# Performance work log

Hardware: AMD Instinct MI355X
Metric: run time of the kernel (lower is better)

The kernel has to match this reference:

```python
import jax, jax.numpy as jnp
import numpy as np

D = 256
N = 1024
L = 6
H = 4
NAMES = ['self', 'cross', 'self', 'cross', 'self', 'cross']


def setup_inputs() -> dict:
    key = jax.random.key(0)
    ks = jax.random.split(key, 12)
    f32 = jnp.float32
    s = D ** -0.5
    s2 = (2 * D) ** -0.5
    return {
        'desc0': jax.random.normal(ks[0], (1, D, N), f32),
        'desc1': jax.random.normal(ks[1], (1, D, N), f32),
        'desc2': jax.random.normal(ks[2], (1, D, N), f32),
        'desc3': jax.random.normal(ks[3], (1, D, N), f32),
        'dist': jax.random.uniform(ks[4], (1, N, N), f32),
        'unreachable': jnp.zeros((N, N), dtype=bool),
        'fidx': jax.random.randint(ks[5], (N, 2), 0, 100),
        'lmb': jax.random.randint(ks[6], (8, 4), 0, 100),
        'proj_w': jax.random.normal(ks[7], (3, L, 3, D, D), f32) * s,
        'proj_b': jnp.zeros((3, L, 3, D), f32),
        'merge_w': jax.random.normal(ks[8], (3, L, D, D), f32) * s,
        'merge_b': jnp.zeros((3, L, D), f32),
        'mlp_w1': jax.random.normal(ks[9], (3, L, 2 * D, 2 * D), f32) * s2,
        'mlp_b1': jnp.zeros((3, L, 2 * D), f32),
        'mlp_w2': jax.random.normal(ks[10], (3, L, D, 2 * D), f32) * s2,
        'mlp_b2': jnp.zeros((3, L, D), f32),
        'norm_g': jnp.ones((4, L, D), f32),
        'norm_b': jnp.zeros((4, L, D), f32),
    }


def _conv(w, b, x):
    # Conv1d kernel_size=1 == per-position linear over channel dim. x: [1, Cin, N]
    return jnp.einsum('od,bdn->bon', w, x) + b[None, :, None]


def _ln(x, g, b):
    # torch does LayerNorm(D) on x.transpose(1,2); equivalent to normalizing channel dim of [1, D, N]
    mu = jnp.mean(x, axis=1, keepdims=True)
    var = jnp.var(x, axis=1, keepdims=True)
    xn = (x - mu) * jax.lax.rsqrt(var + 1e-5)
    return xn * g[None, :, None] + b[None, :, None]


def _mha(pw, pb, mw, mb, q, k, v):
    # pw: [3, D, D], pb: [3, D]; q/k/v: [1, D, Nq/Nk/Nk]; mask is always None in this model
    dh = D // H
    qh = _conv(pw[0], pb[0], q).reshape(1, dh, H, -1)  # [1, dh, H, Nq]
    kh = _conv(pw[1], pb[1], k).reshape(1, dh, H, -1)
    vh = _conv(pw[2], pb[2], v).reshape(1, dh, H, -1)
    scores = jnp.einsum('bdhn,bdhm->bhnm', qh, kh) / jnp.asarray(dh, q.dtype) ** 0.5
    prob = jax.nn.softmax(scores, axis=-1)
    x = jnp.einsum('bhnm,bdhm->bdhn', prob, vh)  # [1, dh, H, Nq]
    out = _conv(mw, mb, x.reshape(1, D, -1))
    return out, scores.mean(axis=1)  # weights: [1, Nq, Nk]


def reference(desc0, desc1, desc2, desc3, dist, unreachable, fidx, lmb,
              proj_w, proj_b, merge_w, merge_b, mlp_w1, mlp_b1, mlp_w2, mlp_b2,
              norm_g, norm_b):
    # ablation == 0 path; dist, fidx, lmb feed dead code in the original forward.
    def prop(br, i, x, src):
        msg, wts = _mha(proj_w[br, i], proj_b[br, i], merge_w[br, i], merge_b[br, i], x, src, src)
        h = jnp.concatenate([x, msg], axis=1)  # [1, 2D, N]
        h = jax.nn.relu(_conv(mlp_w1[br, i], mlp_b1[br, i], h))
        return _conv(mlp_w2[br, i], mlp_b2[br, i], h), wts

    d0, d1, d2, d3 = desc0, desc1, desc2, desc3
    score1 = None
    for i, name in enumerate(NAMES):
        if name == 'cross':
            src0, src1 = d1, d0
        else:
            src0, src1 = d0, d1
        delta0, _ = prop(0, i, d0, src0)
        delta1, score1 = prop(0, i, d1, src1)
        if name == 'cross':
            delta21, _ = prop(1, i, d2, d1)
            delta12, _ = prop(1, i, d1, d2)
            d2 = _ln(d2 + delta21, norm_g[2, i], norm_b[2, i])
            delta03, _ = prop(2, i, d0, d3)
            delta30, _ = prop(2, i, d3, d0)
            d3 = _ln(d3 + delta30, norm_g[3, i], norm_b[3, i])
            d0 = d0 + delta0 + delta03
            d1 = d1 + delta1 + delta12
        else:
            delta2, _ = prop(1, i, d2, d2)
            d2 = _ln(d2 + delta2, norm_g[2, i], norm_b[2, i])
            delta3, _ = prop(2, i, d3, d3)
            d3 = _ln(d3 + delta3, norm_g[3, i], norm_b[3, i])
            d0 = d0 + delta0
            d1 = d1 + delta1
        d0 = _ln(d0, norm_g[0, i], norm_b[0, i])
        d1 = _ln(d1, norm_g[1, i], norm_b[1, i])

    scores = score1.mean(axis=1).reshape(-1)  # [N0]
    unreachable_frontiers = jnp.any(unreachable, axis=0)  # [N0]
    return jnp.where(unreachable_frontiers, jnp.asarray(-1e9, scores.dtype), scores)
```

## Files before the change

kernel.cpp:

```cpp
#include <hip/hip_runtime.h>

#define D 256
#define NPTS 1024
#define H 4
#define LNUM 6

static constexpr size_t SL = (size_t)D * NPTS;

typedef __attribute__((ext_vector_type(8))) short bf16x8;
typedef __attribute__((ext_vector_type(4))) float f32x4;

__device__ __forceinline__ unsigned f2bf(float f) {
  unsigned u = __float_as_uint(f);
  return (u + 0x7FFFu + ((u >> 16) & 1u)) >> 16;
}
__device__ __forceinline__ unsigned pack2(float a, float b) {
  return f2bf(a) | (f2bf(b) << 16);
}
__device__ __forceinline__ float bf2f(unsigned u) {
  return __uint_as_float(u << 16);
}
__device__ __forceinline__ int swz(int row, int byteInRow) {
  return row * 128 + (byteInRow ^ ((row & 7) << 4));
}

struct MMArgs {
  const unsigned short* X[18];
  const unsigned short* X2[18];
  const unsigned short* W[18];
  const float* B[18];
  void* O[18];
};

template <bool RELU>
__global__ __launch_bounds__(256) void mm_bf16(MMArgs a, int K, int xs, int os,
                                               int mode0, int qkv, int split) {
  const int z = blockIdx.z;
  const unsigned short* __restrict__ X = a.X[z];
  const unsigned short* __restrict__ X2 = a.X2[z];
  const unsigned short* __restrict__ W = a.W[z];
  const float* __restrict__ Bb = a.B[z];

  int mode = mode0, osz = os;
  if (qkv && (z % 3 == 2)) { mode = 2; osz = 1024; }
  const float osc = (qkv && (z % 3 == 0)) ? 0.125f : 1.0f;

  __shared__ char sm[64 * 68 * 4];
  char* smX = sm;
  char* smW = sm + 8192;

  const int tid = threadIdx.x;
  const int n0 = blockIdx.x * 64, m0 = blockIdx.y * 64;
  const int lane = tid & 63, wid = tid >> 6;

  f32x4 acc[4] = {{0.f, 0.f, 0.f, 0.f}, {0.f, 0.f, 0.f, 0.f},
                  {0.f, 0.f, 0.f, 0.f}, {0.f, 0.f, 0.f, 0.f}};

  const int srow = tid >> 3, skb = (tid & 7) * 16;
  const int ar = wid * 16 + (lane & 15);
  const int kh = (lane >> 4) * 16;

  for (int k0 = 0; k0 < K; k0 += 64) {
    const int kw = k0 + (skb >> 1);
    int kx = kw;
    const unsigned short* xsrc = X;
    if (split && kx >= split) { xsrc = X2; kx -= split; }
#pragma unroll
    for (int p = 0; p < 2; ++p) {
      const int row = srow + 32 * p;
      *(float4*)(smX + swz(row, skb)) =
          *(const float4*)(xsrc + (size_t)(n0 + row) * xs + kx);
      *(float4*)(smW + swz(row, skb)) =
          *(const float4*)(W + (size_t)(m0 + row) * K + kw);
    }
    __syncthreads();
    const bf16x8 a0 = *(const bf16x8*)(smX + swz(ar, kh));
    const bf16x8 a1 = *(const bf16x8*)(smX + swz(ar, 64 + kh));
#pragma unroll
    for (int c = 0; c < 4; ++c) {
      const int br = c * 16 + (lane & 15);
      const bf16x8 b0 = *(const bf16x8*)(smW + swz(br, kh));
      const bf16x8 b1 = *(const bf16x8*)(smW + swz(br, 64 + kh));
      acc[c] = __builtin_amdgcn_mfma_f32_16x16x32_bf16(a0, b0, acc[c], 0, 0, 0);
      acc[c] = __builtin_amdgcn_mfma_f32_16x16x32_bf16(a1, b1, acc[c], 0, 0, 0);
    }
    __syncthreads();
  }

  float(*eps)[68] = (float(*)[68])sm;
#pragma unroll
  for (int c = 0; c < 4; ++c) {
    const float bs = Bb[m0 + c * 16 + (lane & 15)];
#pragma unroll
    for (int r = 0; r < 4; ++r) {
      float v = (acc[c][r] + bs) * osc;
      if (RELU) v = fmaxf(v, 0.f);
      eps[wid * 16 + (lane >> 4) * 4 + r][c * 16 + (lane & 15)] = v;
    }
  }
  __syncthreads();

#pragma unroll
  for (int p = 0; p < 2; ++p) {
    const int row = srow + 32 * p;
    const int c0 = (tid & 7) * 8;
    if (mode == 0) {
      const float4 lo = *(const float4*)&eps[row][c0];
      const float4 hi = *(const float4*)&eps[row][c0 + 4];
      uint4 u = {pack2(lo.x, lo.y), pack2(lo.z, lo.w), pack2(hi.x, hi.y), pack2(hi.z, hi.w)};
      *(uint4*)((unsigned short*)a.O[z] + (size_t)(n0 + row) * osz + m0 + c0) = u;
    } else if (mode == 1) {
      float* O = (float*)a.O[z];
      *(float4*)(O + (size_t)(n0 + row) * osz + m0 + c0) = *(const float4*)&eps[row][c0];
      *(float4*)(O + (size_t)(n0 + row) * osz + m0 + c0 + 4) = *(const float4*)&eps[row][c0 + 4];
    } else {
      float v[8];
#pragma unroll
      for (int j = 0; j < 8; ++j) v[j] = eps[c0 + j][row];
      uint4 u = {pack2(v[0], v[1]), pack2(v[2], v[3]), pack2(v[4], v[5]), pack2(v[6], v[7])};
      *(uint4*)((unsigned short*)a.O[z] + (size_t)(m0 + row) * osz + n0 + c0) = u;
    }
  }
}

struct AttnArgs {
  const unsigned short* Q[6];
  const unsigned short* K[6];
  const unsigned short* V[6];
};

__global__ __launch_bounds__(256) void attn_split(AttnArgs a, unsigned short* part) {
  const int z = blockIdx.z;
  const int h = blockIdx.y >> 2, ck = blockIdx.y & 3;
  const int n0 = blockIdx.x * 64;
  const unsigned short* __restrict__ Qp = a.Q[z];
  const unsigned short* __restrict__ Kp = a.K[z];
  const unsigned short* __restrict__ Vp = a.V[z];

  __shared__ char sm[49152];
  char* smQ = sm;
  char* smKb = sm + 8192;
  char* smVb = sm + 24576;
  char* smP = sm + 40960;

  const int tid = threadIdx.x;
  const int lane = tid & 63, wid = tid >> 6;
  const int srow = tid >> 2, skb = (tid & 3) * 16;
  const int kb0 = ck * 256;

#pragma unroll
  for (int p = 0; p < 2; ++p) {
    const int b = skb + 64 * p;
    *(float4*)(smQ + swz(srow, b)) =
        *(const float4*)(Qp + (size_t)(n0 + srow) * 256 + h * 64 + (b >> 1));
    *(float4*)(smKb + swz(srow, b)) =
        *(const float4*)(Kp + (size_t)(kb0 + srow) * 256 + h * 64 + (b >> 1));
    *(float4*)(smVb + swz(srow, b)) =
        *(const float4*)(Vp + (size_t)(h * 64 + srow) * NPTS + kb0 + (b >> 1));
  }
  __syncthreads();

  const int kh = (lane >> 4) * 16;
  const int qr = wid * 16 + (lane & 15);
  const bf16x8 qb0 = *(const bf16x8*)(smQ + swz(qr, kh));
  const bf16x8 qb1 = *(const bf16x8*)(smQ + swz(qr, 64 + kh));

  f32x4 accO[4] = {{0.f, 0.f, 0.f, 0.f}, {0.f, 0.f, 0.f, 0.f},
                   {0.f, 0.f, 0.f, 0.f}, {0.f, 0.f, 0.f, 0.f}};
  float mrun = -1e30f, lrun = 0.f;

  for (int t = 0; t < 4; ++t) {
    const int co = (t & 1) << 13;
    if (t < 3) {
      const int no = ((t + 1) & 1) << 13;
      const int kt = kb0 + (t + 1) * 64;
#pragma unroll
      for (int p = 0; p < 2; ++p) {
        const int b = skb + 64 * p;
        *(float4*)(smKb + no + swz(srow, b)) =
            *(const float4*)(Kp + (size_t)(kt + srow) * 256 + h * 64 + (b >> 1));
        *(float4*)(smVb + no + swz(srow, b)) =
            *(const float4*)(Vp + (size_t)(h * 64 + srow) * NPTS + kt + (b >> 1));
      }
    }

    f32x4 s[4];
#pragma unroll
    for (int c = 0; c < 4; ++c) {
      const int br = c * 16 + (lane & 15);
      const bf16x8 kf0 = *(const bf16x8*)(smKb + co + swz(br, kh));
      const bf16x8 kf1 = *(const bf16x8*)(smKb + co + swz(br, 64 + kh));
      f32x4 tt = {0.f, 0.f, 0.f, 0.f};
      tt = __builtin_amdgcn_mfma_f32_16x16x32_bf16(kf0, qb0, tt, 0, 0, 0);
      tt = __builtin_amdgcn_mfma_f32_16x16x32_bf16(kf1, qb1, tt, 0, 0, 0);
      s[c] = tt;
    }

    float mx = s[0][0];
#pragma unroll
    for (int c = 0; c < 4; ++c)
#pragma unroll
      for (int r = 0; r < 4; ++r) mx = fmaxf(mx, s[c][r]);
    mx = fmaxf(mx, __shfl_xor(mx, 16));
    mx = fmaxf(mx, __shfl_xor(mx, 32));
    const float mn = fmaxf(mrun, mx);
    const float corr = __expf(mrun - mn);
    mrun = mn;
    float ps = 0.f;
#pragma unroll
    for (int c = 0; c < 4; ++c)
#pragma unroll
      for (int r = 0; r < 4; ++r) {
        const float e = __expf(s[c][r] - mn);
        s[c][r] = e;
        ps += e;
      }
    ps += __shfl_xor(ps, 16);
    ps += __shfl_xor(ps, 32);
    lrun = lrun * corr + ps;

#pragma unroll
    for (int c = 0; c < 4; ++c) {
      uint2 u;
      u.x = pack2(s[c][0], s[c][1]);
      u.y = pack2(s[c][2], s[c][3]);
      *(uint2*)(smP + swz(qr, c * 32 + (lane >> 4) * 8)) = u;
    }

#pragma unroll
    for (int r = 0; r < 4; ++r) {
      const float cr = __shfl(corr, ((lane >> 4) & 3) * 4 + r);
#pragma unroll
      for (int c = 0; c < 4; ++c) accO[c][r] *= cr;
    }

    const bf16x8 pa0 = *(const bf16x8*)(smP + swz(qr, kh));
    const bf16x8 pa1 = *(const bf16x8*)(smP + swz(qr, 64 + kh));
#pragma unroll
    for (int c = 0; c < 4; ++c) {
      const int vr = c * 16 + (lane & 15);
      const bf16x8 vb0 = *(const bf16x8*)(smVb + co + swz(vr, kh));
      const bf16x8 vb1 = *(const bf16x8*)(smVb + co + swz(vr, 64 + kh));
      accO[c] = __builtin_amdgcn_mfma_f32_16x16x32_bf16(pa0, vb0, accO[c], 0, 0, 0);
      accO[c] = __builtin_amdgcn_mfma_f32_16x16x32_bf16(pa1, vb1, accO[c], 0, 0, 0);
    }
    __syncthreads();
  }

  char* rec = (char*)part +
              (size_t)((((z * 4 + h) * 16 + blockIdx.x) * 4 + ck)) * 8704;
#pragma unroll
  for (int c = 0; c < 4; ++c)
#pragma unroll
    for (int r = 0; r < 4; ++r) {
      const float o0 = accO[c][r];
      const float o1 = __shfl_xor(o0, 1);
      if (!(lane & 1)) {
        const int row = wid * 16 + (lane >> 4) * 4 + r;
        const int col = c * 16 + (lane & 15);
        *(unsigned*)(rec + row * 128 + col * 2) = pack2(o0, o1);
      }
    }
  if (lane < 16) {
    *(float*)(rec + 8192 + (wid * 16 + lane) * 4) = mrun;
    *(float*)(rec + 8448 + (wid * 16 + lane) * 4) = lrun;
  }
}

struct CmbArgs {
  unsigned short* O[6];
};

__global__ __launch_bounds__(256) void attn_combine(CmbArgs a,
                                                    const unsigned short* part) {
  const int z = blockIdx.z, h = blockIdx.y, qb = blockIdx.x;
  const int tid = threadIdx.x;
  const int q = tid >> 2, t4 = tid & 3;
  const char* base = (const char*)part + (size_t)(((z * 4 + h) * 16 + qb) * 4) * 8704;

  float m[4], l[4];
#pragma unroll
  for (int i = 0; i < 4; ++i) {
    m[i] = *(const float*)(base + i * 8704 + 8192 + q * 4);
    l[i] = *(const float*)(base + i * 8704 + 8448 + q * 4);
  }
  const float M = fmaxf(fmaxf(m[0], m[1]), fmaxf(m[2], m[3]));
  float w[4], L = 0.f;
#pragma unroll
  for (int i = 0; i < 4; ++i) { w[i] = __expf(m[i] - M); L += w[i] * l[i]; }
  const float invL = 1.f / L;

  float o[16] = {};
#pragma unroll
  for (int i = 0; i < 4; ++i) {
    const char* Or = base + i * 8704 + q * 128 + t4 * 32;
    unsigned ua[8];
    *(uint4*)ua = *(const uint4*)Or;
    *(uint4*)(ua + 4) = *(const uint4*)(Or + 16);
#pragma unroll
    for (int j = 0; j < 8; ++j) {
      o[2 * j] += w[i] * bf2f(ua[j] & 0xFFFFu);
      o[2 * j + 1] += w[i] * bf2f(ua[j] >> 16);
    }
  }
  unsigned ou[8];
#pragma unroll
  for (int j = 0; j < 8; ++j) ou[j] = pack2(o[2 * j] * invL, o[2 * j + 1] * invL);
  unsigned short* Op = a.O[z] + (size_t)(qb * 64 + q) * 256 + h * 64 + t4 * 16;
  *(uint4*)Op = *(uint4*)ou;
  *(uint4*)(Op + 8) = *(uint4*)(ou + 4);
}

struct LnArgs {
  float* x[4];
  unsigned short* xb[4];
  const float* da[4];
  const float* db[4];
  const float* g[4];
  const float* b[4];
};

__global__ __launch_bounds__(256) void ln_rows(LnArgs a) {
  const int z = blockIdx.z;
  float* __restrict__ x = a.x[z];
  unsigned short* __restrict__ xb = a.xb[z];
  const float* __restrict__ da = a.da[z];
  const float* __restrict__ db = a.db[z];
  const float* __restrict__ g = a.g[z];
  const float* __restrict__ b = a.b[z];

  const int lane = threadIdx.x & 63, wid = threadIdx.x >> 6;
  const int n = blockIdx.x * 4 + wid;
  const size_t off = (size_t)n * 256 + lane * 4;

  float4 v = *(const float4*)(x + off);
  if (da) {
    const float4 w = *(const float4*)(da + off);
    v.x += w.x; v.y += w.y; v.z += w.z; v.w += w.w;
  }
  if (db) {
    const float4 w = *(const float4*)(db + off);
    v.x += w.x; v.y += w.y; v.z += w.z; v.w += w.w;
  }
  float s = v.x + v.y + v.z + v.w;
  float q = v.x * v.x + v.y * v.y + v.z * v.z + v.w * v.w;
#pragma unroll
  for (int o = 1; o < 64; o <<= 1) {
    s += __shfl_xor(s, o);
    q += __shfl_xor(q, o);
  }
  const float mu = s * (1.f / 256.f);
  const float var = q * (1.f / 256.f) - mu * mu;
  const float inv = rsqrtf(var + 1e-5f);
  const float4 gv = *(const float4*)(g + lane * 4);
  const float4 bv = *(const float4*)(b + lane * 4);
  float4 o;
  o.x = (v.x - mu) * inv * gv.x + bv.x;
  o.y = (v.y - mu) * inv * gv.y + bv.y;
  o.z = (v.z - mu) * inv * gv.z + bv.z;
  o.w = (v.w - mu) * inv * gv.w + bv.w;
  *(float4*)(x + off) = o;
  uint2 pk = {pack2(o.x, o.y), pack2(o.z, o.w)};
  *(uint2*)(xb + off) = pk;
}

struct TrArgs {
  const float* s[4];
  float* d[4];
  unsigned short* db[4];
};
__global__ __launch_bounds__(256) void tr_init(TrArgs a) {
  const int z = blockIdx.z;
  const int n0 = blockIdx.x * 64, c0 = blockIdx.y * 64;
  __shared__ float T[64][65];
  const int tid = threadIdx.x;
#pragma unroll
  for (int p = 0; p < 4; ++p) {
    const int row = (tid >> 4) + 16 * p;
    const int col4 = (tid & 15) * 4;
    const float4 v = *(const float4*)(a.s[z] + (size_t)(c0 + row) * NPTS + n0 + col4);
    T[row][col4] = v.x; T[row][col4 + 1] = v.y; T[row][col4 + 2] = v.z; T[row][col4 + 3] = v.w;
  }
  __syncthreads();
#pragma unroll
  for (int p = 0; p < 4; ++p) {
    const int nr = (tid >> 4) + 16 * p;
    const int c4 = (tid & 15) * 4;
    float4 v;
    v.x = T[c4][nr]; v.y = T[c4 + 1][nr]; v.z = T[c4 + 2][nr]; v.w = T[c4 + 3][nr];
    *(float4*)(a.d[z] + (size_t)(n0 + nr) * 256 + c0 + c4) = v;
    uint2 pk = {pack2(v.x, v.y), pack2(v.z, v.w)};
    *(uint2*)(a.db[z] + (size_t)(n0 + nr) * 256 + c0 + c4) = pk;
  }
}

__global__ __launch_bounds__(256) void wp_qkv(const float* __restrict__ pw,
                                              const float* __restrict__ pb,
                                              unsigned short* __restrict__ wbf,
                                              float* __restrict__ pbias) {
  const int z = blockIdx.z;
  const int pi = z / 3, j = z % 3;
  const int br = pi / 5, i = pi % 5;
  const float* src = pw + (((size_t)br * LNUM + i) * 3 + j) * 65536;
  unsigned short* dst = wbf + (size_t)pi * 655360 + (size_t)j * 65536;
  const int t = blockIdx.x * 256 + threadIdx.x;
  const int mp = t >> 6, k4 = (t & 63) * 4;
  const int m = (mp & 63) * 4 + (mp >> 6);
  const float4 v = *(const float4*)(src + (size_t)m * 256 + k4);
  uint2 pk = {pack2(v.x, v.y), pack2(v.z, v.w)};
  *(uint2*)(dst + (size_t)mp * 256 + k4) = pk;
  if (blockIdx.x == 0) {
    const float* sb = pb + (((size_t)br * LNUM + i) * 3 + j) * 256;
    const int mb = threadIdx.x;
    pbias[(size_t)z * 256 + mb] = sb[(mb & 63) * 4 + (mb >> 6)];
  }
}

__global__ __launch_bounds__(256) void wp_mwt(const float* __restrict__ mw,
                                              unsigned short* __restrict__ wbf,
                                              float* __restrict__ zb) {
  const int pi = blockIdx.z;
  const int br = pi / 5, i = pi % 5;
  const float* src = mw + ((size_t)br * LNUM + i) * 65536;
  unsigned short* dst = wbf + (size_t)pi * 655360 + 196608;
  const int t = blockIdx.x * 256 + threadIdx.x;
  const int cp = t >> 6, m4 = (t & 63) * 4;
  const int c = (cp & 63) * 4 + (cp >> 6);
  float v[4];
#pragma unroll
  for (int u = 0; u < 4; ++u) v[u] = src[(size_t)(m4 + u) * 256 + c];
  uint2 pk = {pack2(v[0], v[1]), pack2(v[2], v[3])};
  *(uint2*)(dst + (size_t)cp * 256 + m4) = pk;
  if (blockIdx.x == 0 && pi == 0) zb[threadIdx.x] = 0.f;
}

__global__ __launch_bounds__(256) void wp_c1(const float* __restrict__ w1,
                                             unsigned short* __restrict__ wbf,
                                             unsigned short* __restrict__ whi) {
  const int pi = blockIdx.z;
  const int br = pi / 5, i = pi % 5;
  const float* src = w1 + ((size_t)br * LNUM + i) * 262144;
  unsigned short* dst = wbf + (size_t)pi * 655360 + 262144;
  const int t = blockIdx.x * 256 + threadIdx.x;
  const float4 v = *(const float4*)(src + (size_t)t * 4);
  uint2 pk = {pack2(v.x, v.y), pack2(v.z, v.w)};
  *(uint2*)(dst + (size_t)t * 4) = pk;
  const int idx = t * 4, row = idx >> 9, col = idx & 511;
  if (col >= 256)
    *(uint2*)(whi + (size_t)pi * 131072 + (size_t)row * 256 + (col - 256)) = pk;
}

__global__ __launch_bounds__(256) void wp_c2(const float* __restrict__ w2,
                                             unsigned short* __restrict__ wbf) {
  const int pi = blockIdx.z;
  const int br = pi / 5, i = pi % 5;
  const float* src = w2 + ((size_t)br * LNUM + i) * 131072;
  unsigned short* dst = wbf + (size_t)pi * 655360 + 524288;
  const int t = blockIdx.x * 256 + threadIdx.x;
  const float4 v = *(const float4*)(src + (size_t)t * 4);
  uint2 pk = {pack2(v.x, v.y), pack2(v.z, v.w)};
  *(uint2*)(dst + (size_t)t * 4) = pk;
}

__global__ __launch_bounds__(256) void b1fold(const float* __restrict__ w1,
                                              const float* __restrict__ mb,
                                              const float* __restrict__ b1,
                                              float* __restrict__ out) {
  const int pi = blockIdx.z;
  const int br = pi / 5, i = pi % 5;
  const float* Wp = w1 + ((size_t)br * LNUM + i) * 262144;
  const float* Bp = mb + ((size_t)br * LNUM + i) * 256;
  const float* b1s = b1 + ((size_t)br * LNUM + i) * 512;
  __shared__ float mbs[256];
  mbs[threadIdx.x] = Bp[threadIdx.x];
  __syncthreads();
  for (int o = threadIdx.x; o < 512; o += 256) {
    float s = b1s[o];
    const float* Wr = Wp + (size_t)o * 512 + 256;
#pragma unroll 4
    for (int m = 0; m < 256; ++m) s = fmaf(Wr[m], mbs[m], s);
    out[(size_t)pi * 512 + o] = s;
  }
}

__device__ __forceinline__ float block_reduce_sum(float v) {
  __shared__ float smr[4];
  const int lane = threadIdx.x & 63, wid = threadIdx.x >> 6;
#pragma unroll
  for (int off = 32; off; off >>= 1) v += __shfl_xor(v, off);
  if (lane == 0) smr[wid] = v;
  __syncthreads();
  if (threadIdx.x == 0) v = smr[0] + smr[1] + smr[2] + smr[3];
  return v;
}

__global__ __launch_bounds__(256) void cs1(const float* __restrict__ X,
                                           float* __restrict__ part) {
  const int r0 = blockIdx.x * 64;
  float acc = 0.f;
  for (int r = 0; r < 64; ++r) acc += X[(size_t)(r0 + r) * 256 + threadIdx.x];
  part[(size_t)blockIdx.x * 256 + threadIdx.x] = acc;
}
__global__ __launch_bounds__(256) void cs2(const float* __restrict__ part,
                                           float* __restrict__ s1) {
  float acc = 0.f;
  for (int b = 0; b < 16; ++b) acc += part[(size_t)b * 256 + threadIdx.x];
  s1[threadIdx.x] = acc;
}
__global__ __launch_bounds__(256) void matvec_qbar(const float* __restrict__ Wq,
                                                   const float* __restrict__ bq,
                                                   const float* __restrict__ s1,
                                                   float* __restrict__ qbar) {
  const int d = blockIdx.x, t = threadIdx.x;
  float s = Wq[(size_t)d * 256 + t] * s1[t];
  s = block_reduce_sum(s);
  if (t == 0) qbar[d] = s + (float)NPTS * bq[d];
}
__global__ __launch_bounds__(256) void matvec_u(const float* __restrict__ Wk,
                                                const float* __restrict__ bk,
                                                const float* __restrict__ qbar,
                                                float* __restrict__ u) {
  const int c = blockIdx.x, t = threadIdx.x;
  float s = (c < 256) ? (Wk[(size_t)t * 256 + c] * qbar[t]) : (bk[t] * qbar[t]);
  s = block_reduce_sum(s);
  if (t == 0) u[c] = s;
}

__global__ __launch_bounds__(256) void ur_or(const unsigned* __restrict__ U,
                                             unsigned* __restrict__ part) {
  const int b = blockIdx.x;
  unsigned o = 0;
  for (int r = 0; r < 16; ++r) o |= U[(size_t)(b * 16 + r) * 256 + threadIdx.x];
  part[(size_t)b * 256 + threadIdx.x] = o;
}

__global__ __launch_bounds__(256) void final2(const float* __restrict__ d0,
                                              const float* __restrict__ u,
                                              const unsigned* __restrict__ part,
                                              float* __restrict__ out) {
  const int lane = threadIdx.x & 63, wid = threadIdx.x >> 6;
  const int m = blockIdx.x * 4 + wid;
  const float4 v = *(const float4*)(d0 + (size_t)m * 256 + lane * 4);
  const float4 uu = *(const float4*)(u + lane * 4);
  float s = v.x * uu.x + v.y * uu.y + v.z * uu.z + v.w * uu.w;
  unsigned f = part[(size_t)lane * 256 + (m >> 2)];
  f = (f >> ((m & 3) * 8)) & 0xFFu;
#pragma unroll
  for (int o = 32; o; o >>= 1) {
    s += __shfl_xor(s, o);
    f |= (unsigned)__shfl_xor((int)f, o);
  }
  if (lane == 0) out[m] = f ? -1e9f : (s + u[256]) * (1.f / 32768.f);
}

extern "C" void kernel_launch(void* const* d_in, const int* in_sizes, int n_in,
                              void* d_out, int out_size, void* d_ws, size_t ws_size,
                              hipStream_t stream) {
  const float* desc[4] = {(const float*)d_in[0], (const float*)d_in[1],
                          (const float*)d_in[2], (const float*)d_in[3]};
  const unsigned char* unreach = (const unsigned char*)d_in[5];
  const float* proj_w = (const float*)d_in[8];
  const float* proj_b = (const float*)d_in[9];
  const float* merge_w = (const float*)d_in[10];
  const float* merge_b = (const float*)d_in[11];
  const float* mlp_w1 = (const float*)d_in[12];
  const float* mlp_b1 = (const float*)d_in[13];
  const float* mlp_w2 = (const float*)d_in[14];
  const float* mlp_b2 = (const float*)d_in[15];
  const float* norm_g = (const float*)d_in[16];
  const float* norm_b = (const float*)d_in[17];
  float* out = (float*)d_out;

  float* ws = (float*)d_ws;
  float* dbufF[4];
  for (int t = 0; t < 4; ++t) dbufF[t] = ws + (size_t)t * SL;
  unsigned short* dbfB[4];
  for (int t = 0; t < 4; ++t) dbfB[t] = (unsigned short*)(ws + 4 * SL) + (size_t)t * SL;
  float* deltaF[6];
  for (int p = 0; p < 6; ++p) deltaF[p] = ws + 6 * SL + (size_t)p * SL;
  unsigned short* wbf = (unsigned short*)(ws + 12 * SL);
  float* pbias = ws + 12 * SL + 4915200;
  unsigned* urpart = (unsigned*)(pbias + 11520);
  float* cspart = pbias + 11520 + 16384;
  float* s1 = cspart + 4096;
  float* qbar = s1 + 256;
  float* uvec = qbar + 256;
  float* b1prime = uvec + 260;
  float* zbias = b1prime + 7680;
  unsigned short* attnpart = (unsigned short*)(ws + 12 * SL + 4915200 + 40960);
  unsigned short* whi = attnpart + (size_t)2 * 3342336;
  const size_t base_f = 12 * SL + 4915200 + 40960 + 3342336 + 983040;
  long long avail = (long long)(ws_size / 4) - (long long)base_f;
  const size_t SET_US = 4 * SL;
  int nsets = (int)(avail / (long long)(SET_US / 2));
  if (nsets > 6) nsets = 6;
  if (nsets < 1) nsets = 1;
  unsigned short* usBase = (unsigned short*)(ws + base_f);
  auto setQ = [&](int p) { return usBase + (size_t)p * SET_US; };
  auto setK = [&](int p) { return usBase + (size_t)p * SET_US + SL; };
  auto setV = [&](int p) { return usBase + (size_t)p * SET_US + 2 * SL; };
  auto setO = [&](int p) { return usBase + (size_t)p * SET_US + 3 * SL; };
  auto setH1 = [&](int p) { return usBase + (size_t)p * SET_US; };

  ur_or<<<dim3(64), 256, 0, stream>>>((const unsigned*)unreach, urpart);
  wp_qkv<<<dim3(64, 1, 45), 256, 0, stream>>>(proj_w, proj_b, wbf, pbias);
  wp_mwt<<<dim3(64, 1, 15), 256, 0, stream>>>(merge_w, wbf, zbias);
  wp_c1<<<dim3(256, 1, 15), 256, 0, stream>>>(mlp_w1, wbf, whi);
  wp_c2<<<dim3(128, 1, 15), 256, 0, stream>>>(mlp_w2, wbf);
  b1fold<<<dim3(1, 1, 15), 256, 0, stream>>>(mlp_w1, merge_b, mlp_b1, b1prime);
  {
    MMArgs m{};
    for (int pi = 0; pi < 15; ++pi) {
      const unsigned short* xw = whi + (size_t)pi * 131072;
      m.X[pi] = xw; m.X2[pi] = xw;
      m.W[pi] = wbf + (size_t)pi * 655360 + 196608;
      m.B[pi] = zbias;
      m.O[pi] = wbf + (size_t)pi * 655360 + 262144 + 256;
    }
    mm_bf16<false><<<dim3(8, 4, 15), 256, 0, stream>>>(m, 256, 256, 512, 0, 0, 0);
  }
  {
    TrArgs ta{};
    for (int t = 0; t < 4; ++t) { ta.s[t] = desc[t]; ta.d[t] = dbufF[t]; ta.db[t] = dbfB[t]; }
    tr_init<<<dim3(16, 4, 4), 256, 0, stream>>>(ta);
  }

  static const int selfp[4][3] = {{0, 0, 0}, {0, 1, 1}, {1, 2, 2}, {2, 3, 3}};
  static const int crossp[6][3] = {{0, 0, 1}, {0, 1, 0}, {1, 2, 1},
                                   {1, 1, 2}, {2, 0, 3}, {2, 3, 0}};

  for (int i = 0; i < 5; ++i) {
    const bool cross = (i & 1);
    const int np = cross ? 6 : 4;
    const int(*props)[3] = cross ? crossp : selfp;

    for (int p0 = 0; p0 < np; p0 += nsets) {
      const int g = (np - p0 < nsets) ? (np - p0) : nsets;

      {
        MMArgs m{};
        for (int p = 0; p < g; ++p) {
          const int br = props[p0 + p][0], xi = props[p0 + p][1], si = props[p0 + p][2];
          const int pi = br * 5 + i;
          unsigned short* wb = wbf + (size_t)pi * 655360;
          const unsigned short* xq = dbfB[xi];
          const unsigned short* xsv = dbfB[si];
          m.X[p * 3 + 0] = xq; m.X2[p * 3 + 0] = xq; m.W[p * 3 + 0] = wb;
          m.B[p * 3 + 0] = pbias + ((size_t)pi * 3 + 0) * 256; m.O[p * 3 + 0] = setQ(p);
          m.X[p * 3 + 1] = xsv; m.X2[p * 3 + 1] = xsv; m.W[p * 3 + 1] = wb + 65536;
          m.B[p * 3 + 1] = pbias + ((size_t)pi * 3 + 1) * 256; m.O[p * 3 + 1] = setK(p);
          m.X[p * 3 + 2] = xsv; m.X2[p * 3 + 2] = xsv; m.W[p * 3 + 2] = wb + 131072;
          m.B[p * 3 + 2] = pbias + ((size_t)pi * 3 + 2) * 256; m.O[p * 3 + 2] = setV(p);
        }
        mm_bf16<false><<<dim3(16, 4, 3 * g), 256, 0, stream>>>(m, 256, 256, 256, 0, 1, 0);
      }
      {
        AttnArgs aa{};
        for (int p = 0; p < g; ++p) {
          aa.Q[p] = setQ(p); aa.K[p] = setK(p); aa.V[p] = setV(p);
        }
        attn_split<<<dim3(16, 16, g), 256, 0, stream>>>(aa, attnpart);
        CmbArgs cc{};
        for (int p = 0; p < g; ++p) cc.O[p] = setO(p);
        attn_combine<<<dim3(16, 4, g), 256, 0, stream>>>(cc, attnpart);
      }
      {
        MMArgs m{};
        for (int p = 0; p < g; ++p) {
          const int br = props[p0 + p][0], xi = props[p0 + p][1];
          const int pi = br * 5 + i;
          m.X[p] = dbfB[xi]; m.X2[p] = setO(p);
          m.W[p] = wbf + (size_t)pi * 655360 + 262144;
          m.B[p] = b1prime + (size_t)pi * 512; m.O[p] = setH1(p);
        }
        mm_bf16<true><<<dim3(16, 8, g), 256, 0, stream>>>(m, 512, 256, 512, 0, 0, 256);
      }
      {
        MMArgs m{};
        for (int p = 0; p < g; ++p) {
          const int br = props[p0 + p][0];
          const int pi = br * 5 + i;
          m.X[p] = setH1(p); m.X2[p] = setH1(p);
          m.W[p] = wbf + (size_t)pi * 655360 + 524288;
          m.B[p] = mlp_b2 + ((size_t)br * LNUM + i) * 256; m.O[p] = deltaF[p0 + p];
        }
        mm_bf16<false><<<dim3(16, 4, g), 256, 0, stream>>>(m, 512, 512, 256, 1, 0, 0);
      }
    }

    {
      LnArgs la{};
      for (int t = 0; t < 4; ++t) {
        la.x[t] = dbufF[t]; la.xb[t] = dbfB[t];
        const float* da = nullptr;
        const float* db2 = nullptr;
        for (int p = 0; p < np; ++p)
          if (props[p][1] == t) {
            if (!da) da = deltaF[p];
            else db2 = deltaF[p];
          }
        la.da[t] = da; la.db[t] = db2;
        la.g[t] = norm_g + ((size_t)t * LNUM + i) * 256;
        la.b[t] = norm_b + ((size_t)t * LNUM + i) * 256;
      }
      ln_rows<<<dim3(256, 1, 4), 256, 0, stream>>>(la);
    }
  }

  const float* Wq5 = proj_w + (((size_t)0 * LNUM + 5) * 3 + 0) * 65536;
  const float* bq5 = proj_b + (((size_t)0 * LNUM + 5) * 3 + 0) * 256;
  const float* Wk5 = proj_w + (((size_t)0 * LNUM + 5) * 3 + 1) * 65536;
  const float* bk5 = proj_b + (((size_t)0 * LNUM + 5) * 3 + 1) * 256;

  cs1<<<dim3(16), 256, 0, stream>>>(dbufF[1], cspart);
  cs2<<<dim3(1), 256, 0, stream>>>(cspart, s1);
  matvec_qbar<<<dim3(256), 256, 0, stream>>>(Wq5, bq5, s1, qbar);
  matvec_u<<<dim3(257), 256, 0, stream>>>(Wk5, bk5, qbar, uvec);
  final2<<<dim3(256), 256, 0, stream>>>(dbufF[0], uvec, urpart, out);

  (void)in_sizes; (void)n_in; (void)out_size;
}
```

Baseline: 328.2 us.

## Enlarge GEMM tile to 128 rows and double-buffer LDS with register prefetch

The bf16 MFMA GEMM tile grows from 64x64 to 128x64. Each wave now computes two 16-row blocks, so every B fragment loaded from LDS feeds twice as many MFMAs. The k-loop becomes double-buffered: the next tile is fetched from global memory into registers while the current one is computed, then written to the other LDS buffer, leaving one barrier per iteration. This halves the grid size of every launch, which cuts parallelism for these small GEMMs (N=1024) and raises LDS use to 48KB, possibly lowering occupancy.

```diff
diff --git a/kernel.cpp b/kernel.cpp
--- a/kernel.cpp
+++ b/kernel.cpp
@@ -45,45 +45,68 @@
   if (qkv && (z % 3 == 2)) { mode = 2; osz = 1024; }
   const float osc = (qkv && (z % 3 == 0)) ? 0.125f : 1.0f;
 
-  __shared__ char sm[64 * 68 * 4];
-  char* smX = sm;
-  char* smW = sm + 8192;
+  __shared__ char sm[49152];
 
   const int tid = threadIdx.x;
-  const int n0 = blockIdx.x * 64, m0 = blockIdx.y * 64;
+  const int n0 = blockIdx.x * 128, m0 = blockIdx.y * 64;
   const int lane = tid & 63, wid = tid >> 6;
 
-  f32x4 acc[4] = {{0.f, 0.f, 0.f, 0.f}, {0.f, 0.f, 0.f, 0.f},
-                  {0.f, 0.f, 0.f, 0.f}, {0.f, 0.f, 0.f, 0.f}};
-
-  const int srow = tid >> 3, skb = (tid & 7) * 16;
-  const int ar = wid * 16 + (lane & 15);
+  const int arow = tid >> 1, acb = (tid & 1) * 64;
+  const int brow = tid >> 2, bcb = (tid & 3) * 32;
+
+  f32x4 acc[2][4] = {};
+  float4 ra[4], rb[2];
+
+  auto ldTile = [&](int k0) {
+#pragma unroll
+    for (int j = 0; j < 4; ++j) {
+      int ke = k0 + (acb >> 1) + j * 8;
+      const unsigned short* xsrc = X;
+      if (split && ke >= split) { xsrc = X2; ke -= split; }
+      ra[j] = *(const float4*)(xsrc + (size_t)(n0 + arow) * xs + ke);
+    }
+#pragma unroll
+    for (int j = 0; j < 2; ++j)
+      rb[j] = *(const float4*)(W + (size_t)(m0 + brow) * K + k0 + (bcb >> 1) + j * 8);
+  };
+  auto stTile = [&](int buf) {
+    char* A = sm + buf * 24576;
+    char* B = sm + buf * 24576 + 16384;
+#pragma unroll
+    for (int j = 0; j < 4; ++j) *(float4*)(A + swz(arow, acb + j * 16)) = ra[j];
+#pragma unroll
+    for (int j = 0; j < 2; ++j) *(float4*)(B + swz(brow, bcb + j * 16)) = rb[j];
+  };
+
+  ldTile(0);
+  stTile(0);
+  __syncthreads();
+
   const int kh = (lane >> 4) * 16;
-
-  for (int k0 = 0; k0 < K; k0 += 64) {
-    const int kw = k0 + (skb >> 1);
-    int kx = kw;
-    const unsigned short* xsrc = X;
-    if (split && kx >= split) { xsrc = X2; kx -= split; }
-#pragma unroll
-    for (int p = 0; p < 2; ++p) {
-      const int row = srow + 32 * p;
-      *(float4*)(smX + swz(row, skb)) =
-          *(const float4*)(xsrc + (size_t)(n0 + row) * xs + kx);
-      *(float4*)(smW + swz(row, skb)) =
-          *(const float4*)(W + (size_t)(m0 + row) * K + kw);
-    }
-    __syncthreads();
-    const bf16x8 a0 = *(const bf16x8*)(smX + swz(ar, kh));
-    const bf16x8 a1 = *(const bf16x8*)(smX + swz(ar, 64 + kh));
+  const int r0 = wid * 32 + (lane & 15);
+  const int nit = K >> 6;
+
+  for (int it = 0; it < nit; ++it) {
+    const int cur = it & 1;
+    if (it + 1 < nit) ldTile((it + 1) * 64);
+
+    char* A = sm + cur * 24576;
+    char* B = sm + cur * 24576 + 16384;
+    const bf16x8 a00 = *(const bf16x8*)(A + swz(r0, kh));
+    const bf16x8 a01 = *(const bf16x8*)(A + swz(r0, 64 + kh));
+    const bf16x8 a10 = *(const bf16x8*)(A + swz(r0 + 16, kh));
+    const bf16x8 a11 = *(const bf16x8*)(A + swz(r0 + 16, 64 + kh));
 #pragma unroll
     for (int c = 0; c < 4; ++c) {
       const int br = c * 16 + (lane & 15);
-      const bf16x8 b0 = *(const bf16x8*)(smW + swz(br, kh));
-      const bf16x8 b1 = *(const bf16x8*)(smW + swz(br, 64 + kh));
-      acc[c] = __builtin_amdgcn_mfma_f32_16x16x32_bf16(a0, b0, acc[c], 0, 0, 0);
-      acc[c] = __builtin_amdgcn_mfma_f32_16x16x32_bf16(a1, b1, acc[c], 0, 0, 0);
-    }
+      const bf16x8 b0 = *(const bf16x8*)(B + swz(br, kh));
+      const bf16x8 b1 = *(const bf16x8*)(B + swz(br, 64 + kh));
+      acc[0][c] = __builtin_amdgcn_mfma_f32_16x16x32_bf16(a00, b0, acc[0][c], 0, 0, 0);
+      acc[0][c] = __builtin_amdgcn_mfma_f32_16x16x32_bf16(a01, b1, acc[0][c], 0, 0, 0);
+      acc[1][c] = __builtin_amdgcn_mfma_f32_16x16x32_bf16(a10, b0, acc[1][c], 0, 0, 0);
+      acc[1][c] = __builtin_amdgcn_mfma_f32_16x16x32_bf16(a11, b1, acc[1][c], 0, 0, 0);
+    }
+    if (it + 1 < nit) stTile(cur ^ 1);
     __syncthreads();
   }
 
@@ -92,33 +115,48 @@
   for (int c = 0; c < 4; ++c) {
     const float bs = Bb[m0 + c * 16 + (lane & 15)];
 #pragma unroll
-    for (int r = 0; r < 4; ++r) {
-      float v = (acc[c][r] + bs) * osc;
-      if (RELU) v = fmaxf(v, 0.f);
-      eps[wid * 16 + (lane >> 4) * 4 + r][c * 16 + (lane & 15)] = v;
-    }
+    for (int ri = 0; ri < 2; ++ri)
+#pragma unroll
+      for (int r = 0; r < 4; ++r) {
+        float v = (acc[ri][c][r] + bs) * osc;
+        if (RELU) v = fmaxf(v, 0.f);
+        eps[wid * 32 + ri * 16 + (lane >> 4) * 4 + r][c * 16 + (lane & 15)] = v;
+      }
   }
   __syncthreads();
 
-#pragma unroll
-  for (int p = 0; p < 2; ++p) {
-    const int row = srow + 32 * p;
-    const int c0 = (tid & 7) * 8;
-    if (mode == 0) {
+  if (mode == 0) {
+#pragma unroll
+    for (int p = 0; p < 4; ++p) {
+      const int row = (tid >> 3) + 32 * p;
+      const int c0 = (tid & 7) * 8;
       const float4 lo = *(const float4*)&eps[row][c0];
       const float4 hi = *(const float4*)&eps[row][c0 + 4];
       uint4 u = {pack2(lo.x, lo.y), pack2(lo.z, lo.w), pack2(hi.x, hi.y), pack2(hi.z, hi.w)};
       *(uint4*)((unsigned short*)a.O[z] + (size_t)(n0 + row) * osz + m0 + c0) = u;
-    } else if (mode == 1) {
-      float* O = (float*)a.O[z];
+    }
+  } else if (mode == 1) {
+    float* O = (float*)a.O[z];
+#pragma unroll
+    for (int p = 0; p < 4; ++p) {
+      const int row = (tid >> 3) + 32 * p;
+      const int c0 = (tid & 7) * 8;
       *(float4*)(O + (size_t)(n0 + row) * osz + m0 + c0) = *(const float4*)&eps[row][c0];
       *(float4*)(O + (size_t)(n0 + row) * osz + m0 + c0 + 4) = *(const float4*)&eps[row][c0 + 4];
-    } else {
-      float v[8];
-#pragma unroll
-      for (int j = 0; j < 8; ++j) v[j] = eps[c0 + j][row];
-      uint4 u = {pack2(v[0], v[1]), pack2(v[2], v[3]), pack2(v[4], v[5]), pack2(v[6], v[7])};
-      *(uint4*)((unsigned short*)a.O[z] + (size_t)(m0 + row) * osz + n0 + c0) = u;
+    }
+  } else {
+#pragma unroll
+    for (int p = 0; p < 2; ++p) {
+      const int mrow = (tid >> 3) + 32 * p;
+      const int nc0 = (tid & 7) * 16;
+      float v[16];
+#pragma unroll
+      for (int j = 0; j < 16; ++j) v[j] = eps[nc0 + j][mrow];
+      uint4 u0 = {pack2(v[0], v[1]), pack2(v[2], v[3]), pack2(v[4], v[5]), pack2(v[6], v[7])};
+      uint4 u1 = {pack2(v[8], v[9]), pack2(v[10], v[11]), pack2(v[12], v[13]), pack2(v[14], v[15])};
+      unsigned short* Op = (unsigned short*)a.O[z] + (size_t)(m0 + mrow) * osz + n0 + nc0;
+      *(uint4*)Op = u0;
+      *(uint4*)(Op + 8) = u1;
     }
   }
 }
@@ -617,7 +655,7 @@
       m.B[pi] = zbias;
       m.O[pi] = wbf + (size_t)pi * 655360 + 262144 + 256;
     }
-    mm_bf16<false><<<dim3(8, 4, 15), 256, 0, stream>>>(m, 256, 256, 512, 0, 0, 0);
+    mm_bf16<false><<<dim3(4, 4, 15), 256, 0, stream>>>(m, 256, 256, 512, 0, 0, 0);
   }
   {
     TrArgs ta{};
@@ -652,7 +690,7 @@
           m.X[p * 3 + 2] = xsv; m.X2[p * 3 + 2] = xsv; m.W[p * 3 + 2] = wb + 131072;
           m.B[p * 3 + 2] = pbias + ((size_t)pi * 3 + 2) * 256; m.O[p * 3 + 2] = setV(p);
         }
-        mm_bf16<false><<<dim3(16, 4, 3 * g), 256, 0, stream>>>(m, 256, 256, 256, 0, 1, 0);
+        mm_bf16<false><<<dim3(8, 4, 3 * g), 256, 0, stream>>>(m, 256, 256, 256, 0, 1, 0);
       }
       {
         AttnArgs aa{};
@@ -673,7 +711,7 @@
           m.W[p] = wbf + (size_t)pi * 655360 + 262144;
           m.B[p] = b1prime + (size_t)pi * 512; m.O[p] = setH1(p);
         }
-        mm_bf16<true><<<dim3(16, 8, g), 256, 0, stream>>>(m, 512, 256, 512, 0, 0, 256);
+        mm_bf16<true><<<dim3(8, 8, g), 256, 0, stream>>>(m, 512, 256, 512, 0, 0, 256);
       }
       {
         MMArgs m{};
@@ -684,7 +722,7 @@
           m.W[p] = wbf + (size_t)pi * 655360 + 524288;
           m.B[p] = mlp_b2 + ((size_t)br * LNUM + i) * 256; m.O[p] = deltaF[p0 + p];
         }
-        mm_bf16<false><<<dim3(16, 4, g), 256, 0, stream>>>(m, 512, 512, 256, 1, 0, 0);
+        mm_bf16<false><<<dim3(8, 4, g), 256, 0, stream>>>(m, 512, 512, 256, 1, 0, 0);
       }
     }
 
```

After: 523.4 us. 59.5% more time.

## Enlarge GEMM tiles to 128x128 with 4x4 MFMA per wave and direct epilogue

Applied to the files above, without the earlier changes.

Changes the bf16 MFMA GEMM from 64x64 block tiles to 128x128 tiles. Each wave now computes a 64x64 sub-tile with 16 accumulators, reusing A fragments across four B columns. The epilogue no longer stages through LDS: results are packed with lane shuffles and written straight to global memory. The goal is more reuse and less LDS traffic, but the grid shrinks fourfold, which can leave many CUs idle on these small GEMMs.

```diff
diff --git a/kernel.cpp b/kernel.cpp
--- a/kernel.cpp
+++ b/kernel.cpp
@@ -45,80 +45,101 @@
   if (qkv && (z % 3 == 2)) { mode = 2; osz = 1024; }
   const float osc = (qkv && (z % 3 == 0)) ? 0.125f : 1.0f;
 
-  __shared__ char sm[64 * 68 * 4];
-  char* smX = sm;
-  char* smW = sm + 8192;
+  __shared__ char sm[32768];
+  char* smA = sm;
+  char* smB = sm + 16384;
 
   const int tid = threadIdx.x;
-  const int n0 = blockIdx.x * 64, m0 = blockIdx.y * 64;
+  const int n0 = blockIdx.x * 128, m0 = blockIdx.y * 128;
   const int lane = tid & 63, wid = tid >> 6;
-
-  f32x4 acc[4] = {{0.f, 0.f, 0.f, 0.f}, {0.f, 0.f, 0.f, 0.f},
-                  {0.f, 0.f, 0.f, 0.f}, {0.f, 0.f, 0.f, 0.f}};
-
-  const int srow = tid >> 3, skb = (tid & 7) * 16;
-  const int ar = wid * 16 + (lane & 15);
-  const int kh = (lane >> 4) * 16;
+  const int wr = wid >> 1, wc = wid & 1;
+  const int lr = lane & 15, lk = lane >> 4;
+  const int kh = lk * 16;
+
+  const int srow = tid >> 1, sc4 = (tid & 1) * 4;
+
+  f32x4 acc[4][4] = {};
 
   for (int k0 = 0; k0 < K; k0 += 64) {
-    const int kw = k0 + (skb >> 1);
-    int kx = kw;
-    const unsigned short* xsrc = X;
-    if (split && kx >= split) { xsrc = X2; kx -= split; }
-#pragma unroll
-    for (int p = 0; p < 2; ++p) {
-      const int row = srow + 32 * p;
-      *(float4*)(smX + swz(row, skb)) =
-          *(const float4*)(xsrc + (size_t)(n0 + row) * xs + kx);
-      *(float4*)(smW + swz(row, skb)) =
-          *(const float4*)(W + (size_t)(m0 + row) * K + kw);
+#pragma unroll
+    for (int j = 0; j < 4; ++j) {
+      const int ck = sc4 + j;
+      const int ke = k0 + ck * 8;
+      int kx = ke;
+      const unsigned short* xsrc = X;
+      if (split && kx >= split) { xsrc = X2; kx -= split; }
+      *(float4*)(smA + swz(srow, ck * 16)) =
+          *(const float4*)(xsrc + (size_t)(n0 + srow) * xs + kx);
+      *(float4*)(smB + swz(srow, ck * 16)) =
+          *(const float4*)(W + (size_t)(m0 + srow) * K + ke);
     }
     __syncthreads();
-    const bf16x8 a0 = *(const bf16x8*)(smX + swz(ar, kh));
-    const bf16x8 a1 = *(const bf16x8*)(smX + swz(ar, 64 + kh));
-#pragma unroll
-    for (int c = 0; c < 4; ++c) {
-      const int br = c * 16 + (lane & 15);
-      const bf16x8 b0 = *(const bf16x8*)(smW + swz(br, kh));
-      const bf16x8 b1 = *(const bf16x8*)(smW + swz(br, 64 + kh));
-      acc[c] = __builtin_amdgcn_mfma_f32_16x16x32_bf16(a0, b0, acc[c], 0, 0, 0);
-      acc[c] = __builtin_amdgcn_mfma_f32_16x16x32_bf16(a1, b1, acc[c], 0, 0, 0);
+
+    bf16x8 af[4][2];
+#pragma unroll
+    for (int ri = 0; ri < 4; ++ri) {
+      const int ar = wr * 64 + ri * 16 + lr;
+      af[ri][0] = *(const bf16x8*)(smA + swz(ar, kh));
+      af[ri][1] = *(const bf16x8*)(smA + swz(ar, 64 + kh));
+    }
+#pragma unroll
+    for (int ci = 0; ci < 4; ++ci) {
+      const int br = wc * 64 + ci * 16 + lr;
+      const bf16x8 b0 = *(const bf16x8*)(smB + swz(br, kh));
+      const bf16x8 b1 = *(const bf16x8*)(smB + swz(br, 64 + kh));
+#pragma unroll
+      for (int ri = 0; ri < 4; ++ri) {
+        acc[ri][ci] = __builtin_amdgcn_mfma_f32_16x16x32_bf16(af[ri][0], b0, acc[ri][ci], 0, 0, 0);
+        acc[ri][ci] = __builtin_amdgcn_mfma_f32_16x16x32_bf16(af[ri][1], b1, acc[ri][ci], 0, 0, 0);
+      }
     }
     __syncthreads();
   }
 
-  float(*eps)[68] = (float(*)[68])sm;
-#pragma unroll
-  for (int c = 0; c < 4; ++c) {
-    const float bs = Bb[m0 + c * 16 + (lane & 15)];
-#pragma unroll
-    for (int r = 0; r < 4; ++r) {
-      float v = (acc[c][r] + bs) * osc;
-      if (RELU) v = fmaxf(v, 0.f);
-      eps[wid * 16 + (lane >> 4) * 4 + r][c * 16 + (lane & 15)] = v;
-    }
-  }
-  __syncthreads();
-
-#pragma unroll
-  for (int p = 0; p < 2; ++p) {
-    const int row = srow + 32 * p;
-    const int c0 = (tid & 7) * 8;
-    if (mode == 0) {
-      const float4 lo = *(const float4*)&eps[row][c0];
-      const float4 hi = *(const float4*)&eps[row][c0 + 4];
-      uint4 u = {pack2(lo.x, lo.y), pack2(lo.z, lo.w), pack2(hi.x, hi.y), pack2(hi.z, hi.w)};
-      *(uint4*)((unsigned short*)a.O[z] + (size_t)(n0 + row) * osz + m0 + c0) = u;
-    } else if (mode == 1) {
-      float* O = (float*)a.O[z];
-      *(float4*)(O + (size_t)(n0 + row) * osz + m0 + c0) = *(const float4*)&eps[row][c0];
-      *(float4*)(O + (size_t)(n0 + row) * osz + m0 + c0 + 4) = *(const float4*)&eps[row][c0 + 4];
-    } else {
-      float v[8];
-#pragma unroll
-      for (int j = 0; j < 8; ++j) v[j] = eps[c0 + j][row];
-      uint4 u = {pack2(v[0], v[1]), pack2(v[2], v[3]), pack2(v[4], v[5]), pack2(v[6], v[7])};
-      *(uint4*)((unsigned short*)a.O[z] + (size_t)(m0 + row) * osz + n0 + c0) = u;
+#pragma unroll
+  for (int ci = 0; ci < 4; ++ci) {
+    const int col = wc * 64 + ci * 16 + lr;
+    const float bs = Bb[m0 + col];
+#pragma unroll
+    for (int ri = 0; ri < 4; ++ri) {
+      const int rowb = wr * 64 + ri * 16 + lk * 4;
+      float v[4];
+#pragma unroll
+      for (int r = 0; r < 4; ++r) {
+        float t = (acc[ri][ci][r] + bs) * osc;
+        if (RELU) t = fmaxf(t, 0.f);
+        v[r] = t;
+      }
+      if (mode == 2) {
+        uint2 u;
+        u.x = pack2(v[0], v[1]);
+        u.y = pack2(v[2], v[3]);
+        *(uint2*)((unsigned short*)a.O[z] + (size_t)(m0 + col) * osz + n0 + rowb) = u;
+      } else if (mode == 0) {
+#pragma unroll
+        for (int r = 0; r < 4; ++r) {
+          const float o1 = __shfl_xor(v[r], 1);
+          const unsigned p01 = pack2(v[r], o1);
+          const unsigned p23 = __shfl_xor((int)p01, 2);
+          if ((lane & 3) == 0) {
+            uint2 u;
+            u.x = p01;
+            u.y = (unsigned)p23;
+            *(uint2*)((unsigned short*)a.O[z] + (size_t)(n0 + rowb + r) * osz + m0 + col) = u;
+          }
+        }
+      } else {
+#pragma unroll
+        for (int r = 0; r < 4; ++r) {
+          const float o1 = __shfl_xor(v[r], 1);
+          if (!(lane & 1)) {
+            float2 u;
+            u.x = v[r];
+            u.y = o1;
+            *(float2*)((float*)a.O[z] + (size_t)(n0 + rowb + r) * osz + m0 + col) = u;
+          }
+        }
+      }
     }
   }
 }
@@ -617,7 +638,7 @@
       m.B[pi] = zbias;
       m.O[pi] = wbf + (size_t)pi * 655360 + 262144 + 256;
     }
-    mm_bf16<false><<<dim3(8, 4, 15), 256, 0, stream>>>(m, 256, 256, 512, 0, 0, 0);
+    mm_bf16<false><<<dim3(4, 2, 15), 256, 0, stream>>>(m, 256, 256, 512, 0, 0, 0);
   }
   {
     TrArgs ta{};
@@ -652,7 +673,7 @@
           m.X[p * 3 + 2] = xsv; m.X2[p * 3 + 2] = xsv; m.W[p * 3 + 2] = wb + 131072;
           m.B[p * 3 + 2] = pbias + ((size_t)pi * 3 + 2) * 256; m.O[p * 3 + 2] = setV(p);
         }
-        mm_bf16<false><<<dim3(16, 4, 3 * g), 256, 0, stream>>>(m, 256, 256, 256, 0, 1, 0);
+        mm_bf16<false><<<dim3(8, 2, 3 * g), 256, 0, stream>>>(m, 256, 256, 256, 0, 1, 0);
       }
       {
         AttnArgs aa{};
@@ -673,7 +694,7 @@
           m.W[p] = wbf + (size_t)pi * 655360 + 262144;
           m.B[p] = b1prime + (size_t)pi * 512; m.O[p] = setH1(p);
         }
-        mm_bf16<true><<<dim3(16, 8, g), 256, 0, stream>>>(m, 512, 256, 512, 0, 0, 256);
+        mm_bf16<true><<<dim3(8, 4, g), 256, 0, stream>>>(m, 512, 256, 512, 0, 0, 256);
       }
       {
         MMArgs m{};
@@ -684,7 +705,7 @@
           m.W[p] = wbf + (size_t)pi * 655360 + 524288;
           m.B[p] = mlp_b2 + ((size_t)br * LNUM + i) * 256; m.O[p] = deltaF[p0 + p];
         }
-        mm_bf16<false><<<dim3(16, 4, g), 256, 0, stream>>>(m, 512, 512, 256, 1, 0, 0);
+        mm_bf16<false><<<dim3(8, 2, g), 256, 0, stream>>>(m, 512, 512, 256, 1, 0, 0);
       }
     }
 
```

After: 509.8 us. 1.55x slower.
